# Optimization experiments

Hardware: AMD Instinct MI355X
Metric: run time of the kernel (lower is better)

The kernel has to match this reference:

```python
import jax, jax.numpy as jnp
import numpy as np

N = 10000
IN_F = 512
OUT_F = 64
ALPHA = 0.2
NEG_INF = -9e15


def setup_inputs() -> dict:
    key = jax.random.key(0)
    k1, k2, k3, k4, k5, k6 = jax.random.split(key, 6)
    x = jax.random.normal(k1, (N, IN_F), dtype=jnp.float32)
    adj = jax.random.randint(k2, (N, N), 0, 2).astype(jnp.float32)
    M = jax.random.uniform(k3, (N, N), dtype=jnp.float32)
    W = jax.random.normal(k4, (IN_F, OUT_F), dtype=jnp.float32) * (1.414 / np.sqrt(IN_F))
    a_self = jax.random.normal(k5, (OUT_F, 1), dtype=jnp.float32) * 0.1
    a_neighs = jax.random.normal(k6, (OUT_F, 1), dtype=jnp.float32) * 0.1
    return {"x": x, "adj": adj, "M": M, "W": W, "a_self": a_self, "a_neighs": a_neighs}


def reference(x, adj, M, W, a_self, a_neighs):
    # h: [N, out_features]
    h = x @ W
    attn_for_self = h @ a_self      # [N, 1]
    attn_for_neighs = h @ a_neighs  # [N, 1]
    # outer-sum broadcast -> [N, N]
    attn_dense = attn_for_self + attn_for_neighs.T
    attn_dense = attn_dense * M
    attn_dense = jax.nn.leaky_relu(attn_dense, negative_slope=ALPHA)
    scores = jnp.where(adj > 0, attn_dense, NEG_INF)
    attention = jax.nn.softmax(scores, axis=1)
    h_prime = attention @ h  # [N, out_features]
    return jax.nn.elu(h_prime)  # concat=True path
```

## Files before the change

### kernel.cpp

```cpp
#include <hip/hip_runtime.h>
#include <math.h>

#define Nn 10000
#define NPAD 10048
#define INF_ 512
#define OUTF 64
#define ALPHA 0.2f
#define LOG2E 1.4426950408889634f

#define TI 32
#define TJ 64
#define NTILES ((Nn + TJ - 1) / TJ)
#define YS 6
#define TPC ((NTILES + YS - 1) / YS)

typedef __attribute__((ext_vector_type(8))) short bfrag;
typedef __attribute__((ext_vector_type(4))) float facc;

#define WS_S    0
#define WS_T    (Nn)
#define WS_TMAX (2*Nn)
#define WS_DEN  (2*Nn + 16)
#define WS_HP   (WS_DEN + YS*Nn)
#define WS_HBT  (WS_HP + YS*Nn*OUTF)

__device__ __forceinline__ unsigned short f2bf(float f) {
    unsigned int u = __float_as_uint(f);
    u += 0x7fffu + ((u >> 16) & 1u);
    return (unsigned short)(u >> 16);
}
__device__ __forceinline__ unsigned int pk2(float a, float b) {
    return (unsigned int)f2bf(a) | ((unsigned int)f2bf(b) << 16);
}

__global__ __launch_bounds__(256) void hgemm_kernel(
    const float* __restrict__ x, const float* __restrict__ W,
    const float* __restrict__ a_self, const float* __restrict__ a_neighs,
    unsigned short* __restrict__ hbfT, float* __restrict__ s, float* __restrict__ t)
{
    const int col  = threadIdx.x & 63;
    const int wid  = threadIdx.x >> 6;
    const int row0 = blockIdx.x * 16 + wid * 4;
    const float* x0 = x + row0 * INF_;

    float acc0 = 0.f, acc1 = 0.f, acc2 = 0.f, acc3 = 0.f;
    #pragma unroll 4
    for (int k4 = 0; k4 < INF_ / 4; ++k4) {
        const int k = k4 << 2;
        const float w0 = W[(k    ) * OUTF + col];
        const float w1 = W[(k + 1) * OUTF + col];
        const float w2 = W[(k + 2) * OUTF + col];
        const float w3 = W[(k + 3) * OUTF + col];
        const float4 xa = *(const float4*)(x0 +          k);
        const float4 xb = *(const float4*)(x0 +   INF_ + k);
        const float4 xc = *(const float4*)(x0 + 2*INF_ + k);
        const float4 xd = *(const float4*)(x0 + 3*INF_ + k);
        acc0 = fmaf(xa.x,w0, fmaf(xa.y,w1, fmaf(xa.z,w2, fmaf(xa.w,w3, acc0))));
        acc1 = fmaf(xb.x,w0, fmaf(xb.y,w1, fmaf(xb.z,w2, fmaf(xb.w,w3, acc1))));
        acc2 = fmaf(xc.x,w0, fmaf(xc.y,w1, fmaf(xc.z,w2, fmaf(xc.w,w3, acc2))));
        acc3 = fmaf(xd.x,w0, fmaf(xd.y,w1, fmaf(xd.z,w2, fmaf(xd.w,w3, acc3))));
    }
    ushort4 hb;
    hb.x = f2bf(acc0); hb.y = f2bf(acc1); hb.z = f2bf(acc2); hb.w = f2bf(acc3);
    *(ushort4*)(hbfT + (size_t)col * NPAD + row0) = hb;

    const float as = a_self[col], an = a_neighs[col];
    #define RED(ACC, U) { \
        float vs = (ACC) * as, vn = (ACC) * an; \
        _Pragma("unroll") \
        for (int d_ = 32; d_; d_ >>= 1) { vs += __shfl_xor(vs, d_); vn += __shfl_xor(vn, d_); } \
        if (col == 0) { s[row0 + (U)] = vs; t[row0 + (U)] = vn; } }
    RED(acc0, 0) RED(acc1, 1) RED(acc2, 2) RED(acc3, 3)
    #undef RED
}

__global__ __launch_bounds__(1024) void tmax_kernel(
    const float* __restrict__ t, float* __restrict__ tmax)
{
    __shared__ float red[16];
    float m = -3e38f;
    for (int i = threadIdx.x; i < Nn; i += 1024) m = fmaxf(m, t[i]);
    #pragma unroll
    for (int d = 32; d; d >>= 1) m = fmaxf(m, __shfl_xor(m, d));
    if ((threadIdx.x & 63) == 0) red[threadIdx.x >> 6] = m;
    __syncthreads();
    if (threadIdx.x < 16) {
        m = red[threadIdx.x];
        #pragma unroll
        for (int d = 8; d; d >>= 1) m = fmaxf(m, __shfl_xor(m, d));
        if (threadIdx.x == 0) *tmax = m;
    }
}

__global__ __launch_bounds__(256, 6) void gat_main_kernel(
    const float* __restrict__ adj, const float* __restrict__ Mm,
    const unsigned short* __restrict__ hbfT, const float* __restrict__ sv,
    const float* __restrict__ tv, const float* __restrict__ tmaxp,
    float* __restrict__ den_part, float* __restrict__ hp_part)
{
    __shared__ __align__(16) unsigned short hTl[OUTF][TJ + 8];
    __shared__ __align__(16) unsigned short Pl[TI][TJ + 8];

    const int tid = threadIdx.x;
    const int i0  = blockIdx.x * TI;
    const int tlo = blockIdx.y * TPC;
    const int thi = min(NTILES, tlo + TPC);

    const int rr = tid >> 3, jc = tid & 7;
    const int prow = i0 + rr;
    const bool rowok = prow < Nn;
    const float si = rowok ? sv[prow] : 0.0f;
    const float mc = fmaxf(0.0f, si + *tmaxp) * LOG2E;
    const float* aRow = adj + (size_t)prow * Nn;
    const float* mRow = Mm  + (size_t)prow * Nn;

    const int hc_ = tid >> 2, hseg = tid & 3;
    const unsigned short* hsrc = hbfT + (size_t)hc_ * NPAD + hseg * 16;

    const int lane = tid & 63, wv = tid >> 6;
    const int l15 = lane & 15, kq = lane >> 4;
    const int rb = wv & 1, cbp = wv >> 1;
    const unsigned short* aP  = &Pl[rb * 16 + l15][kq * 8];
    const unsigned short* bP0 = &hTl[cbp * 32 + l15][kq * 8];
    const unsigned short* bP1 = bP0 + 16 * (TJ + 8);

    facc accA = {0.f, 0.f, 0.f, 0.f}, accB = {0.f, 0.f, 0.f, 0.f};
    float denacc = 0.0f;

    const float4 z4 = make_float4(0.f, 0.f, 0.f, 0.f);
    float4 pa0 = z4, pa1 = z4, pm0 = z4, pm1 = z4, pt0 = z4, pt1 = z4;
    uint4 ph0 = make_uint4(0,0,0,0), ph1 = make_uint4(0,0,0,0);

    auto prefetch = [&](int tile) {
        const int j0 = tile * TJ;
        ph0 = *(const uint4*)(hsrc + j0);
        ph1 = *(const uint4*)(hsrc + j0 + 8);
        const int jl = j0 + (jc << 3);
        if (rowok && jl + 7 < Nn) {
            pa0 = *(const float4*)(aRow + jl); pa1 = *(const float4*)(aRow + jl + 4);
            pm0 = *(const float4*)(mRow + jl); pm1 = *(const float4*)(mRow + jl + 4);
            pt0 = *(const float4*)(tv   + jl); pt1 = *(const float4*)(tv   + jl + 4);
        } else {
            pa0 = pa1 = pm0 = pm1 = pt0 = pt1 = z4;
            if (rowok) {
                #define LD1(dst, base, off) if ((jl + (off)) < Nn) dst = (base)[jl + (off)]
                LD1(pa0.x, aRow, 0); LD1(pa0.y, aRow, 1); LD1(pa0.z, aRow, 2); LD1(pa0.w, aRow, 3);
                LD1(pa1.x, aRow, 4); LD1(pa1.y, aRow, 5); LD1(pa1.z, aRow, 6); LD1(pa1.w, aRow, 7);
                LD1(pm0.x, mRow, 0); LD1(pm0.y, mRow, 1); LD1(pm0.z, mRow, 2); LD1(pm0.w, mRow, 3);
                LD1(pm1.x, mRow, 4); LD1(pm1.y, mRow, 5); LD1(pm1.z, mRow, 6); LD1(pm1.w, mRow, 7);
                LD1(pt0.x, tv,   0); LD1(pt0.y, tv,   1); LD1(pt0.z, tv,   2); LD1(pt0.w, tv,   3);
                LD1(pt1.x, tv,   4); LD1(pt1.y, tv,   5); LD1(pt1.z, tv,   6); LD1(pt1.w, tv,   7);
                #undef LD1
            }
        }
    };

    #define PC(dst, av, mv, tvv) { \
        float e_ = (si + (tvv)) * (mv); \
        float l_ = fmaxf(e_, ALPHA * e_); \
        dst = ((av) > 0.0f) ? exp2f(fmaf(l_, LOG2E, -mc)) : 0.0f; }

    prefetch(tlo);
    for (int tile = tlo; tile < thi; ++tile) {
        __syncthreads();

        *(uint4*)&hTl[hc_][hseg * 16]     = ph0;
        *(uint4*)&hTl[hc_][hseg * 16 + 8] = ph1;

        float4 p40, p41;
        PC(p40.x, pa0.x, pm0.x, pt0.x); PC(p40.y, pa0.y, pm0.y, pt0.y);
        PC(p40.z, pa0.z, pm0.z, pt0.z); PC(p40.w, pa0.w, pm0.w, pt0.w);
        PC(p41.x, pa1.x, pm1.x, pt1.x); PC(p41.y, pa1.y, pm1.y, pt1.y);
        PC(p41.z, pa1.z, pm1.z, pt1.z); PC(p41.w, pa1.w, pm1.w, pt1.w);
        denacc += ((p40.x + p40.y) + (p40.z + p40.w)) + ((p41.x + p41.y) + (p41.z + p41.w));

        uint4 pw;
        pw.x = pk2(p40.x, p40.y); pw.y = pk2(p40.z, p40.w);
        pw.z = pk2(p41.x, p41.y); pw.w = pk2(p41.z, p41.w);
        *(uint4*)&Pl[rr][jc << 3] = pw;

        __syncthreads();

        if (tile + 1 < thi) prefetch(tile + 1);
        __builtin_amdgcn_sched_barrier(0);

        #pragma unroll
        for (int k0 = 0; k0 < TJ; k0 += 32) {
            const bfrag af = *(const bfrag*)(aP  + k0);
            const bfrag b0 = *(const bfrag*)(bP0 + k0);
            const bfrag b1 = *(const bfrag*)(bP1 + k0);
            accA = __builtin_amdgcn_mfma_f32_16x16x32_bf16(af, b0, accA, 0, 0, 0);
            accB = __builtin_amdgcn_mfma_f32_16x16x32_bf16(af, b1, accB, 0, 0, 0);
        }
    }
    #undef PC

    float d = denacc;
    d += __shfl_xor(d, 1); d += __shfl_xor(d, 2); d += __shfl_xor(d, 4);
    if (rowok && jc == 0) den_part[blockIdx.y * Nn + prow] = d;

    float* hp = hp_part + (size_t)blockIdx.y * (Nn * OUTF);
    const int orow = i0 + rb * 16 + (kq << 2);
    const int oc   = cbp * 32 + l15;
    #pragma unroll
    for (int r = 0; r < 4; ++r) {
        if (orow + r < Nn) {
            hp[(orow + r) * OUTF + oc]      = accA[r];
            hp[(orow + r) * OUTF + oc + 16] = accB[r];
        }
    }
}

__global__ __launch_bounds__(256) void finalize_kernel(
    const float* __restrict__ dp, const float* __restrict__ hp,
    float* __restrict__ out)
{
    const int idx = blockIdx.x * 256 + threadIdx.x;
    const int S = Nn * OUTF;
    const int row = idx >> 6;
    float num = 0.0f, den = 0.0f;
    #pragma unroll
    for (int y = 0; y < YS; ++y) {
        num += hp[(size_t)y * S + idx];
        den += dp[y * Nn + row];
    }
    const float v = num / den;
    out[idx] = (v > 0.0f) ? v : expm1f(v);
}

extern "C" void kernel_launch(void* const* d_in, const int* in_sizes, int n_in,
                              void* d_out, int out_size, void* d_ws, size_t ws_size,
                              hipStream_t stream) {
    const float* x        = (const float*)d_in[0];
    const float* adj      = (const float*)d_in[1];
    const float* Mm       = (const float*)d_in[2];
    const float* W        = (const float*)d_in[3];
    const float* a_self   = (const float*)d_in[4];
    const float* a_neighs = (const float*)d_in[5];

    float* out  = (float*)d_out;
    float* ws   = (float*)d_ws;
    float* s    = ws + WS_S;
    float* t    = ws + WS_T;
    float* tmax = ws + WS_TMAX;
    float* denp = ws + WS_DEN;
    float* hpp  = ws + WS_HP;
    unsigned short* hbfT = (unsigned short*)(ws + WS_HBT);

    hgemm_kernel<<<Nn / 16, 256, 0, stream>>>(x, W, a_self, a_neighs, hbfT, s, t);
    tmax_kernel<<<1, 1024, 0, stream>>>(t, tmax);
    gat_main_kernel<<<dim3((Nn + TI - 1) / TI, YS), 256, 0, stream>>>(
        adj, Mm, hbfT, s, t, tmax, denp, hpp);
    finalize_kernel<<<(Nn * OUTF) / 256, 256, 0, stream>>>(denp, hpp, out);
}
```

Before: 274.4 us.

## Stream adj, M and h tiles into LDS via async global_load_lds double buffering

The main GAT kernel now copies adj, M, the transposed bf16 h tile and t directly from global memory into double-buffered LDS with global_load_lds, instead of loading through registers. The next tile is issued before the current one is computed, with explicit vmcnt waits and raw s_barrier calls, and XOR-swizzled LDS layouts replace row padding to avoid bank conflicts. The goal is to overlap the bandwidth-bound streaming of the two dense N×N matrices with the exp and MFMA work while using fewer registers. In exchange LDS use per block rises sharply, the occupancy hint is dropped, and the hand-counted waitcnt values are fragile. Boundary rows and columns are handled by clamping addresses and zeroing probabilities afterwards.

```diff
diff --git a/kernel.cpp b/kernel.cpp
--- a/kernel.cpp
+++ b/kernel.cpp
@@ -31,6 +31,17 @@
 }
 __device__ __forceinline__ unsigned int pk2(float a, float b) {
     return (unsigned int)f2bf(a) | ((unsigned int)f2bf(b) << 16);
+}
+
+__device__ __forceinline__ void dma16(const void* g, void* l) {
+    __builtin_amdgcn_global_load_lds(
+        (const __attribute__((address_space(1))) void*)g,
+        (__attribute__((address_space(3))) void*)l, 16, 0, 0);
+}
+__device__ __forceinline__ void dma4(const void* g, void* l) {
+    __builtin_amdgcn_global_load_lds(
+        (const __attribute__((address_space(1))) void*)g,
+        (__attribute__((address_space(3))) void*)l, 4, 0, 0);
 }
 
 __global__ __launch_bounds__(256) void hgemm_kernel(
@@ -92,106 +103,142 @@
     }
 }
 
-__global__ __launch_bounds__(256, 6) void gat_main_kernel(
+__global__ __launch_bounds__(256) void gat_main_kernel(
     const float* __restrict__ adj, const float* __restrict__ Mm,
     const unsigned short* __restrict__ hbfT, const float* __restrict__ sv,
     const float* __restrict__ tv, const float* __restrict__ tmaxp,
     float* __restrict__ den_part, float* __restrict__ hp_part)
 {
-    __shared__ __align__(16) unsigned short hTl[OUTF][TJ + 8];
-    __shared__ __align__(16) unsigned short Pl[TI][TJ + 8];
-
-    const int tid = threadIdx.x;
-    const int i0  = blockIdx.x * TI;
-    const int tlo = blockIdx.y * TPC;
-    const int thi = min(NTILES, tlo + TPC);
+    __shared__ __align__(16) float          adjL[2][TI * TJ];
+    __shared__ __align__(16) float          ML  [2][TI * TJ];
+    __shared__ __align__(16) unsigned short hTl [2][OUTF * TJ];
+    __shared__ __align__(16) unsigned short Pl  [TI * TJ];
+    __shared__ __align__(16) float          tLt [2][TJ];
+
+    const int tid  = threadIdx.x;
+    const int i0   = blockIdx.x * TI;
+    const int tlo  = blockIdx.y * TPC;
+    const int thi  = min(NTILES, tlo + TPC);
+    const int lane = tid & 63, wv = tid >> 6;
+
+    const float* aSrc[2]; const float* mSrc[2]; const unsigned short* hSrc[2];
+    int aColG[2], hColG[2];
+    #pragma unroll
+    for (int k = 0; k < 2; ++k) {
+        const int p  = (wv * 2 + k) * 64 + lane;
+        const int r  = p >> 4, cp = p & 15;
+        aColG[k] = ((cp ^ (r & 7)) << 2);
+        const int row = min(i0 + r, Nn - 1);
+        aSrc[k] = adj + (size_t)row * Nn;
+        mSrc[k] = Mm  + (size_t)row * Nn;
+        const int hr = p >> 3, hcp = p & 7;
+        hColG[k] = ((hcp ^ (hr & 7)) << 3);
+        hSrc[k] = hbfT + (size_t)hr * NPAD;
+    }
+
+    auto stage = [&](int nt, int nb) {
+        const int j0n = nt * TJ;
+        #pragma unroll
+        for (int k = 0; k < 2; ++k) {
+            const int ii = wv * 2 + k;
+            int c = j0n + aColG[k]; c = min(c, Nn - 4);
+            dma16(aSrc[k] + c, &adjL[nb][ii * 256]);
+            dma16(mSrc[k] + c, &ML  [nb][ii * 256]);
+            dma16(hSrc[k] + j0n + hColG[k], &hTl[nb][ii * 512]);
+        }
+        if (wv == 3) dma4(tv + j0n + lane, &tLt[nb][0]);
+    };
 
     const int rr = tid >> 3, jc = tid & 7;
     const int prow = i0 + rr;
     const bool rowok = prow < Nn;
     const float si = rowok ? sv[prow] : 0.0f;
     const float mc = fmaxf(0.0f, si + *tmaxp) * LOG2E;
-    const float* aRow = adj + (size_t)prow * Nn;
-    const float* mRow = Mm  + (size_t)prow * Nn;
-
-    const int hc_ = tid >> 2, hseg = tid & 3;
-    const unsigned short* hsrc = hbfT + (size_t)hc_ * NPAD + hseg * 16;
-
-    const int lane = tid & 63, wv = tid >> 6;
+    const int rsw   = rr & 7;
+    const int aoff0 = rr * 64 + (((2 * jc    ) ^ rsw) << 2);
+    const int aoff1 = rr * 64 + (((2 * jc + 1) ^ rsw) << 2);
+    const int poff  = rr * 64 + ((jc ^ rsw) << 3);
+
     const int l15 = lane & 15, kq = lane >> 4;
     const int rb = wv & 1, cbp = wv >> 1;
-    const unsigned short* aP  = &Pl[rb * 16 + l15][kq * 8];
-    const unsigned short* bP0 = &hTl[cbp * 32 + l15][kq * 8];
-    const unsigned short* bP1 = bP0 + 16 * (TJ + 8);
+    const int ar = rb * 16 + l15;
+    const unsigned short* aPb = &Pl[ar * 64];
+    const int a_k0 = (((kq    ) ^ (ar & 7)) << 3);
+    const int a_k1 = (((kq + 4) ^ (ar & 7)) << 3);
+    const int oc0 = cbp * 32 + l15, oc1 = oc0 + 16;
+    const int osw = oc0 & 7;
+    const int b_k0 = (((kq    ) ^ osw) << 3);
+    const int b_k1 = (((kq + 4) ^ osw) << 3);
 
     facc accA = {0.f, 0.f, 0.f, 0.f}, accB = {0.f, 0.f, 0.f, 0.f};
     float denacc = 0.0f;
-
-    const float4 z4 = make_float4(0.f, 0.f, 0.f, 0.f);
-    float4 pa0 = z4, pa1 = z4, pm0 = z4, pm1 = z4, pt0 = z4, pt1 = z4;
-    uint4 ph0 = make_uint4(0,0,0,0), ph1 = make_uint4(0,0,0,0);
-
-    auto prefetch = [&](int tile) {
-        const int j0 = tile * TJ;
-        ph0 = *(const uint4*)(hsrc + j0);
-        ph1 = *(const uint4*)(hsrc + j0 + 8);
-        const int jl = j0 + (jc << 3);
-        if (rowok && jl + 7 < Nn) {
-            pa0 = *(const float4*)(aRow + jl); pa1 = *(const float4*)(aRow + jl + 4);
-            pm0 = *(const float4*)(mRow + jl); pm1 = *(const float4*)(mRow + jl + 4);
-            pt0 = *(const float4*)(tv   + jl); pt1 = *(const float4*)(tv   + jl + 4);
-        } else {
-            pa0 = pa1 = pm0 = pm1 = pt0 = pt1 = z4;
-            if (rowok) {
-                #define LD1(dst, base, off) if ((jl + (off)) < Nn) dst = (base)[jl + (off)]
-                LD1(pa0.x, aRow, 0); LD1(pa0.y, aRow, 1); LD1(pa0.z, aRow, 2); LD1(pa0.w, aRow, 3);
-                LD1(pa1.x, aRow, 4); LD1(pa1.y, aRow, 5); LD1(pa1.z, aRow, 6); LD1(pa1.w, aRow, 7);
-                LD1(pm0.x, mRow, 0); LD1(pm0.y, mRow, 1); LD1(pm0.z, mRow, 2); LD1(pm0.w, mRow, 3);
-                LD1(pm1.x, mRow, 4); LD1(pm1.y, mRow, 5); LD1(pm1.z, mRow, 6); LD1(pm1.w, mRow, 7);
-                LD1(pt0.x, tv,   0); LD1(pt0.y, tv,   1); LD1(pt0.z, tv,   2); LD1(pt0.w, tv,   3);
-                LD1(pt1.x, tv,   4); LD1(pt1.y, tv,   5); LD1(pt1.z, tv,   6); LD1(pt1.w, tv,   7);
-                #undef LD1
-            }
-        }
-    };
 
     #define PC(dst, av, mv, tvv) { \
         float e_ = (si + (tvv)) * (mv); \
         float l_ = fmaxf(e_, ALPHA * e_); \
         dst = ((av) > 0.0f) ? exp2f(fmaf(l_, LOG2E, -mc)) : 0.0f; }
 
-    prefetch(tlo);
-    for (int tile = tlo; tile < thi; ++tile) {
-        __syncthreads();
-
-        *(uint4*)&hTl[hc_][hseg * 16]     = ph0;
-        *(uint4*)&hTl[hc_][hseg * 16 + 8] = ph1;
+    stage(tlo, 0);
+    int cur = 0;
+    for (int t = tlo; t < thi; ++t) {
+        if (t + 1 < thi) {
+            stage(t + 1, cur ^ 1);
+            if (wv == 3) asm volatile("s_waitcnt vmcnt(7)" ::: "memory");
+            else         asm volatile("s_waitcnt vmcnt(6)" ::: "memory");
+        } else {
+            asm volatile("s_waitcnt vmcnt(0)" ::: "memory");
+        }
+        __builtin_amdgcn_s_barrier();
+        __builtin_amdgcn_sched_barrier(0);
+
+        const float4 a0 = *(const float4*)&adjL[cur][aoff0];
+        const float4 a1 = *(const float4*)&adjL[cur][aoff1];
+        const float4 m0 = *(const float4*)&ML  [cur][aoff0];
+        const float4 m1 = *(const float4*)&ML  [cur][aoff1];
+        const float4 t0 = *(const float4*)&tLt [cur][jc * 8];
+        const float4 t1 = *(const float4*)&tLt [cur][jc * 8 + 4];
 
         float4 p40, p41;
-        PC(p40.x, pa0.x, pm0.x, pt0.x); PC(p40.y, pa0.y, pm0.y, pt0.y);
-        PC(p40.z, pa0.z, pm0.z, pt0.z); PC(p40.w, pa0.w, pm0.w, pt0.w);
-        PC(p41.x, pa1.x, pm1.x, pt1.x); PC(p41.y, pa1.y, pm1.y, pt1.y);
-        PC(p41.z, pa1.z, pm1.z, pt1.z); PC(p41.w, pa1.w, pm1.w, pt1.w);
-        denacc += ((p40.x + p40.y) + (p40.z + p40.w)) + ((p41.x + p41.y) + (p41.z + p41.w));
+        PC(p40.x, a0.x, m0.x, t0.x); PC(p40.y, a0.y, m0.y, t0.y);
+        PC(p40.z, a0.z, m0.z, t0.z); PC(p40.w, a0.w, m0.w, t0.w);
+        PC(p41.x, a1.x, m1.x, t1.x); PC(p41.y, a1.y, m1.y, t1.y);
+        PC(p41.z, a1.z, m1.z, t1.z); PC(p41.w, a1.w, m1.w, t1.w);
+
+        const int j0 = t * TJ;
+        if (j0 + TJ > Nn) {
+            const int jl = j0 + (jc << 3);
+            if (jl + 0 >= Nn) p40.x = 0.f; if (jl + 1 >= Nn) p40.y = 0.f;
+            if (jl + 2 >= Nn) p40.z = 0.f; if (jl + 3 >= Nn) p40.w = 0.f;
+            if (jl + 4 >= Nn) p41.x = 0.f; if (jl + 5 >= Nn) p41.y = 0.f;
+            if (jl + 6 >= Nn) p41.z = 0.f; if (jl + 7 >= Nn) p41.w = 0.f;
+        }
+        denacc += ((p40.x + p40.y) + (p40.z + p40.w))
+                + ((p41.x + p41.y) + (p41.z + p41.w));
 
         uint4 pw;
         pw.x = pk2(p40.x, p40.y); pw.y = pk2(p40.z, p40.w);
         pw.z = pk2(p41.x, p41.y); pw.w = pk2(p41.z, p41.w);
-        *(uint4*)&Pl[rr][jc << 3] = pw;
-
-        __syncthreads();
-
-        if (tile + 1 < thi) prefetch(tile + 1);
+        *(uint4*)&Pl[poff] = pw;
+
+        asm volatile("s_waitcnt lgkmcnt(0)" ::: "memory");
+        __builtin_amdgcn_s_barrier();
         __builtin_amdgcn_sched_barrier(0);
 
-        #pragma unroll
-        for (int k0 = 0; k0 < TJ; k0 += 32) {
-            const bfrag af = *(const bfrag*)(aP  + k0);
-            const bfrag b0 = *(const bfrag*)(bP0 + k0);
-            const bfrag b1 = *(const bfrag*)(bP1 + k0);
-            accA = __builtin_amdgcn_mfma_f32_16x16x32_bf16(af, b0, accA, 0, 0, 0);
-            accB = __builtin_amdgcn_mfma_f32_16x16x32_bf16(af, b1, accB, 0, 0, 0);
-        }
+        const bfrag af0 = *(const bfrag*)&aPb[a_k0];
+        const bfrag af1 = *(const bfrag*)&aPb[a_k1];
+        const unsigned short* H0 = &hTl[cur][oc0 * 64];
+        const unsigned short* H1 = &hTl[cur][oc1 * 64];
+        const bfrag b00 = *(const bfrag*)&H0[b_k0];
+        const bfrag b01 = *(const bfrag*)&H0[b_k1];
+        const bfrag b10 = *(const bfrag*)&H1[b_k0];
+        const bfrag b11 = *(const bfrag*)&H1[b_k1];
+        accA = __builtin_amdgcn_mfma_f32_16x16x32_bf16(af0, b00, accA, 0, 0, 0);
+        accB = __builtin_amdgcn_mfma_f32_16x16x32_bf16(af0, b10, accB, 0, 0, 0);
+        accA = __builtin_amdgcn_mfma_f32_16x16x32_bf16(af1, b01, accA, 0, 0, 0);
+        accB = __builtin_amdgcn_mfma_f32_16x16x32_bf16(af1, b11, accB, 0, 0, 0);
+
+        __builtin_amdgcn_s_barrier();
+        cur ^= 1;
     }
     #undef PC
 
```

After: 264.6 us. 3.6% less time.
